# Kernel tuning notes

Measured on AMD Instinct MI355X. Metric: run time of the kernel, lower is better.

The kernel has to match this reference:

```python
import jax, jax.numpy as jnp
import numpy as np

B, S, D, U = 32, 2048, 1024, 1024


def setup_inputs() -> dict:
    key = jax.random.key(0)
    ks = jax.random.split(key, 8)
    scale_in = 1.0 / np.sqrt(D)
    scale_u = 1.0 / np.sqrt(U)
    return {
        "query": jax.random.normal(ks[0], (B, D), dtype=jnp.float32),
        "values": jax.random.normal(ks[1], (B, S, D), dtype=jnp.float32),
        "W1": jax.random.normal(ks[2], (D, U), dtype=jnp.float32) * scale_in,
        "b1": jnp.zeros((U,), dtype=jnp.float32),
        "W2": jax.random.normal(ks[3], (D, U), dtype=jnp.float32) * scale_in,
        "b2": jnp.zeros((U,), dtype=jnp.float32),
        "V": jax.random.normal(ks[4], (U, 1), dtype=jnp.float32) * scale_u,
        "bV": jnp.zeros((1,), dtype=jnp.float32),
    }


def reference(query, values, W1, b1, W2, b2, V, bV):
    # values: [B, S, D] -> [B, S, U]; query: [B, D] -> [B, 1, U]
    proj_v = jnp.einsum("bsd,du->bsu", values, W1) + b1
    proj_q = (query @ W2 + b2)[:, None, :]
    # score: [B, S, 1]
    score = jnp.einsum("bsu,uo->bso", jnp.tanh(proj_v + proj_q), V) + bV
    attention_weights = jax.nn.softmax(score, axis=1)
    # context: [B, D]
    context_vector = jnp.sum(attention_weights * values, axis=1)
    return (context_vector, attention_weights)
```

## Files before the change

kernel.cpp:

```cpp
#include <hip/hip_runtime.h>

#define DEVFN __device__ __forceinline__
#define GLOBAL_AS __attribute__((address_space(1)))
#define LDS_AS __attribute__((address_space(3)))

typedef __attribute__((ext_vector_type(4))) float f32x4;
typedef __attribute__((ext_vector_type(8))) short short8;
typedef __attribute__((ext_vector_type(8))) unsigned short ushort8;

constexpr int CB = 32;
constexpr int CS = 2048;
constexpr int CD = 1024;
constexpr int CU = 1024;
constexpr int CM = CB * CS;

DEVFN unsigned f2bf_u(float f) {
    unsigned u = __float_as_uint(f);
    return (u + 0x7FFFu + ((u >> 16) & 1u)) >> 16;
}
DEVFN unsigned f2bf_pack(float lo, float hi) {
    return f2bf_u(lo) | (f2bf_u(hi) << 16);
}
DEVFN float tanh_fast(float x) {
    float e = exp2f(x * 2.885390081777927f);
    return 1.0f - 2.0f * __builtin_amdgcn_rcpf(e + 1.0f);
}
DEVFN void async_lds16(const void* g, void* l) {
    __builtin_amdgcn_global_load_lds((const GLOBAL_AS unsigned int*)g,
                                     (LDS_AS unsigned int*)l, 16, 0, 0);
}

__global__ void k_bias1(const float* __restrict__ q, const float* __restrict__ W2,
                        float* __restrict__ bpart) {
    int dc = blockIdx.x, b = blockIdx.y;
    int t = threadIdx.x;
    __shared__ float qs[128];
    if (t < 128) qs[t] = q[b * CD + dc * 128 + t];
    __syncthreads();
    float acc0 = 0.f, acc1 = 0.f, acc2 = 0.f, acc3 = 0.f;
    const float* w2 = W2 + (size_t)(dc * 128) * CU + t;
#pragma unroll 4
    for (int d = 0; d < 128; ++d) {
        float qv = qs[d];
        const float* r = w2 + (size_t)d * CU;
        acc0 += qv * r[0];
        acc1 += qv * r[256];
        acc2 += qv * r[512];
        acc3 += qv * r[768];
    }
    float* o = bpart + (size_t)(b * 8 + dc) * CU + t;
    o[0] = acc0; o[256] = acc1; o[512] = acc2; o[768] = acc3;
}

__global__ void k_bias2(const float* __restrict__ bpart, const float* __restrict__ b1,
                        const float* __restrict__ b2, float* __restrict__ bias) {
    int idx = blockIdx.x * 256 + threadIdx.x;
    int b = idx >> 10, u = idx & 1023;
    float s = b1[u] + b2[u];
#pragma unroll
    for (int dc = 0; dc < 8; ++dc) s += bpart[(size_t)(b * 8 + dc) * CU + u];
    bias[idx] = s;
}

__global__ void k_packW1(const float* __restrict__ W1, unsigned short* __restrict__ W1p) {
    int tid = blockIdx.x * 256 + threadIdx.x;
    int o8  = tid * 8;
    int l   = (o8 >> 3) & 63;
    int ub  = (o8 >> 9) & 15;
    int ut  = (o8 >> 13) & 3;
    int kt  = o8 >> 15;
    int u  = ut * 256 + ub * 16 + (l & 15);
    int d0 = kt * 32 + (l >> 4) * 8;
    ushort8 v;
#pragma unroll
    for (int j = 0; j < 8; ++j)
        v[j] = (unsigned short)f2bf_u(W1[(size_t)(d0 + j) * CU + u]);
    *(ushort8*)(W1p + o8) = v;
}

__global__ __launch_bounds__(512, 2) void k_score(
    const float* __restrict__ values, const unsigned short* __restrict__ W1p,
    const float* __restrict__ bias, const float* __restrict__ V,
    float* __restrict__ score) {
    __shared__ __align__(16) char smem[139264];

    const int t = threadIdx.x;
    const int w = t >> 6, l = t & 63;
    const int w8 = w * 8;
    const int m0 = blockIdx.x * 64;
    const int bb = m0 >> 11;

    const float* aSrcT = values + (size_t)(m0 + (t >> 3)) * CD + (t & 7) * 4;
    const int aWrByte = (t >> 7) * 1024
                      + (((t >> 3) & 15) | (((t >> 1) & 3) << 4)) * 16
                      + (t & 1) * 8;
    const unsigned short* bSrc = W1p + (size_t)w8 * 512 + l * 8;
    const int bRdBase = (w >> 1) * 16384 + (w & 1) * 8192;

    f32x4 zero4 = {0.f, 0.f, 0.f, 0.f};
    f32x4 acc[4][8];
#pragma unroll
    for (int i = 0; i < 4; ++i)
#pragma unroll
        for (int j = 0; j < 8; ++j) acc[i][j] = zero4;

    f32x4 aH0, aH1;

    {
        char* bl = smem + 8192 + w8 * 1024;
#pragma unroll
        for (int q = 0; q < 8; ++q) async_lds16(bSrc + q * 512, bl + q * 1024);
        aH0 = *(const f32x4*)(aSrcT);
        aH1 = *(const f32x4*)(aSrcT + 32);
        uint2 pk;
        pk.x = f2bf_pack(aH0[0], aH0[1]);
        pk.y = f2bf_pack(aH0[2], aH0[3]);
        *(uint2*)(smem + aWrByte) = pk;
    }

#define SCORE_BODY(KT, AH_LD, AH_WR, DO_LD, DO_STAGE, DO_WR)                        \
    {                                                                               \
        const int cur = (KT) & 1, nxt = cur ^ 1;                                    \
        asm volatile("s_waitcnt vmcnt(1)" ::: "memory");                            \
        asm volatile("s_waitcnt lgkmcnt(0)" ::: "memory");                          \
        asm volatile("s_barrier" ::: "memory");                                     \
        __builtin_amdgcn_sched_barrier(0);                                          \
        if (DO_STAGE) {                                                             \
            const unsigned short* bs = bSrc + (size_t)((KT) + 1) * 32768;           \
            char* bl = smem + 8192 + nxt * 65536 + w8 * 1024;                       \
            _Pragma("unroll")                                                       \
            for (int q = 0; q < 8; ++q) async_lds16(bs + q * 512, bl + q * 1024);   \
        }                                                                           \
        if (DO_LD) AH_LD = *(const f32x4*)(aSrcT + ((KT) + 2) * 32);                \
        __builtin_amdgcn_sched_barrier(0);                                          \
        const char* aB = smem + cur * 4096;                                         \
        const char* bB = smem + 8192 + cur * 65536 + bRdBase;                       \
        short8 aF[4], bF[8];                                                        \
        _Pragma("unroll")                                                           \
        for (int i = 0; i < 4; ++i)                                                 \
            aF[i] = *(const short8*)(aB + i * 1024 + l * 16);                       \
        _Pragma("unroll")                                                           \
        for (int j = 0; j < 8; ++j)                                                 \
            bF[j] = *(const short8*)(bB + j * 1024 + l * 16);                       \
        __builtin_amdgcn_s_setprio(1);                                              \
        _Pragma("unroll")                                                           \
        for (int i = 0; i < 4; ++i)                                                 \
            _Pragma("unroll")                                                       \
            for (int j = 0; j < 8; ++j)                                             \
                acc[i][j] = __builtin_amdgcn_mfma_f32_16x16x32_bf16(                \
                    aF[i], bF[j], acc[i][j], 0, 0, 0);                              \
        __builtin_amdgcn_s_setprio(0);                                              \
        __builtin_amdgcn_sched_barrier(0);                                          \
        if (DO_WR) {                                                                \
            uint2 pk;                                                               \
            pk.x = f2bf_pack(AH_WR[0], AH_WR[1]);                                   \
            pk.y = f2bf_pack(AH_WR[2], AH_WR[3]);                                   \
            *(uint2*)(smem + nxt * 4096 + aWrByte) = pk;                            \
        }                                                                           \
    }

    for (int kt = 0; kt < 30; kt += 2) {
        SCORE_BODY(kt,     aH0, aH1, true, true, true)
        SCORE_BODY(kt + 1, aH1, aH0, true, true, true)
    }
    SCORE_BODY(30, aH0, aH1, false, true, true)
    SCORE_BODY(31, aH0, aH0, false, false, false)
#undef SCORE_BODY

    float part[4][4];
#pragma unroll
    for (int i = 0; i < 4; ++i)
#pragma unroll
        for (int rr = 0; rr < 4; ++rr) part[i][rr] = 0.f;

#pragma unroll
    for (int j = 0; j < 8; ++j) {
        int col = w * 128 + j * 16 + (l & 15);
        float vv = V[col];
        float bz = bias[bb * CU + col];
#pragma unroll
        for (int i = 0; i < 4; ++i)
#pragma unroll
            for (int rr = 0; rr < 4; ++rr)
                part[i][rr] += vv * tanh_fast(acc[i][j][rr] + bz);
    }

    __syncthreads();
    float* red = (float*)smem;
#pragma unroll
    for (int i = 0; i < 4; ++i)
#pragma unroll
        for (int rr = 0; rr < 4; ++rr) {
            float v = part[i][rr];
            v += __shfl_xor(v, 1);
            v += __shfl_xor(v, 2);
            v += __shfl_xor(v, 4);
            v += __shfl_xor(v, 8);
            if ((l & 15) == 0)
                red[w * 64 + i * 16 + (l >> 4) * 4 + rr] = v;
        }
    __syncthreads();
    if (t < 64) {
        float s = 0.f;
#pragma unroll
        for (int ww = 0; ww < 8; ++ww) s += red[ww * 64 + t];
        score[m0 + t] = s;
    }
}

__global__ void k_softmax(const float* __restrict__ score, float* __restrict__ wts) {
    int b = blockIdx.x, t = threadIdx.x;
    int i0 = b * CS + t, i1 = i0 + 1024;
    float s0 = score[i0];
    float s1 = score[i1];
    __shared__ float red[16];
    int wv = t >> 6, ln = t & 63;
    float m = fmaxf(s0, s1);
#pragma unroll
    for (int o = 32; o >= 1; o >>= 1) m = fmaxf(m, __shfl_xor(m, o));
    if (ln == 0) red[wv] = m;
    __syncthreads();
    float M = red[0];
#pragma unroll
    for (int k = 1; k < 16; ++k) M = fmaxf(M, red[k]);
    float e0 = __expf(s0 - M), e1 = __expf(s1 - M);
    float sm = e0 + e1;
#pragma unroll
    for (int o = 32; o >= 1; o >>= 1) sm += __shfl_xor(sm, o);
    __syncthreads();
    if (ln == 0) red[wv] = sm;
    __syncthreads();
    float T = 0.f;
#pragma unroll
    for (int k = 0; k < 16; ++k) T += red[k];
    float inv = 1.0f / T;
    wts[i0] = e0 * inv;
    wts[i1] = e1 * inv;
}

__global__ void k_ctx_part(const float* __restrict__ values, const float* __restrict__ wts,
                           float* __restrict__ part) {
    int b = blockIdx.y, sc = blockIdx.x;
    int t = threadIdx.x;
    const float* vb = values + ((size_t)b * CS + sc * 64) * CD + t * 4;
    const float* wb = wts + b * CS + sc * 64;
    f32x4 a = {0.f, 0.f, 0.f, 0.f};
#pragma unroll 8
    for (int s = 0; s < 64; ++s) {
        float wgt = wb[s];
        f32x4 v = *(const f32x4*)(vb + (size_t)s * CD);
        a += v * wgt;
    }
    *(f32x4*)(part + (size_t)(b * 32 + sc) * CD + t * 4) = a;
}

__global__ void k_ctx_red(const float* __restrict__ part, float* __restrict__ ctx) {
    int idx = blockIdx.x * 256 + threadIdx.x;
    int b = idx >> 10, d = idx & 1023;
    float s = 0.f;
#pragma unroll 8
    for (int c = 0; c < 32; ++c) s += part[(size_t)(b * 32 + c) * CD + d];
    ctx[idx] = s;
}

extern "C" void kernel_launch(void* const* d_in, const int* in_sizes, int n_in,
                              void* d_out, int out_size, void* d_ws, size_t ws_size,
                              hipStream_t stream) {
    const float* query  = (const float*)d_in[0];
    const float* values = (const float*)d_in[1];
    const float* W1     = (const float*)d_in[2];
    const float* b1     = (const float*)d_in[3];
    const float* W2     = (const float*)d_in[4];
    const float* b2     = (const float*)d_in[5];
    const float* V      = (const float*)d_in[6];

    float* out = (float*)d_out;
    float* ctx = out;
    float* wts = out + 32768;

    char* ws = (char*)d_ws;
    float*          score = (float*)ws;
    float*          bias  = (float*)(ws + (1 << 20));
    unsigned short* W1p   = (unsigned short*)(ws + (1 << 20) + (1 << 17));
    float*          part  = (float*)(ws + (1 << 20) + (1 << 17) + (1 << 21));
    float*          bpart = part;

    k_bias1<<<dim3(8, 32), 256, 0, stream>>>(query, W2, bpart);
    k_bias2<<<128, 256, 0, stream>>>(bpart, b1, b2, bias);
    k_packW1<<<512, 256, 0, stream>>>(W1, W1p);
    k_score<<<1024, 512, 0, stream>>>(values, W1p, bias, V, score);
    k_softmax<<<32, 1024, 0, stream>>>(score, wts);
    k_ctx_part<<<dim3(32, 32), 256, 0, stream>>>(values, wts, part);
    k_ctx_red<<<128, 256, 0, stream>>>(part, ctx);
}
```

Before: 268.5 us.

## Load W1 fragments directly into registers instead of staging through LDS

The B-operand (packed bf16 W1) fragments are now loaded from global memory straight into double-buffered register arrays, rather than being copied asynchronously into a 128KB LDS double buffer and read back. This shrinks shared memory to 8KB, removes the LDS round trip and the explicit vmcnt waits, and could allow more resident blocks. In exchange, each wave loads its own W1 slice from global/L2 without sharing, register pressure rises from holding two sets of eight short8 fragments, and the compiler now manages the wait counts on the global loads.

```diff
diff --git a/kernel.cpp b/kernel.cpp
--- a/kernel.cpp
+++ b/kernel.cpp
@@ -24,10 +24,6 @@
 DEVFN float tanh_fast(float x) {
     float e = exp2f(x * 2.885390081777927f);
     return 1.0f - 2.0f * __builtin_amdgcn_rcpf(e + 1.0f);
-}
-DEVFN void async_lds16(const void* g, void* l) {
-    __builtin_amdgcn_global_load_lds((const GLOBAL_AS unsigned int*)g,
-                                     (LDS_AS unsigned int*)l, 16, 0, 0);
 }
 
 __global__ void k_bias1(const float* __restrict__ q, const float* __restrict__ W2,
@@ -82,11 +78,10 @@
     const float* __restrict__ values, const unsigned short* __restrict__ W1p,
     const float* __restrict__ bias, const float* __restrict__ V,
     float* __restrict__ score) {
-    __shared__ __align__(16) char smem[139264];
+    __shared__ __align__(16) char smem[8192];
 
     const int t = threadIdx.x;
     const int w = t >> 6, l = t & 63;
-    const int w8 = w * 8;
     const int m0 = blockIdx.x * 64;
     const int bb = m0 >> 11;
 
@@ -94,8 +89,7 @@
     const int aWrByte = (t >> 7) * 1024
                       + (((t >> 3) & 15) | (((t >> 1) & 3) << 4)) * 16
                       + (t & 1) * 8;
-    const unsigned short* bSrc = W1p + (size_t)w8 * 512 + l * 8;
-    const int bRdBase = (w >> 1) * 16384 + (w & 1) * 8192;
+    const unsigned short* bSrc = W1p + (size_t)w * 4096 + l * 8;
 
     f32x4 zero4 = {0.f, 0.f, 0.f, 0.f};
     f32x4 acc[4][8];
@@ -104,67 +98,61 @@
 #pragma unroll
         for (int j = 0; j < 8; ++j) acc[i][j] = zero4;
 
+    short8 bFA[8], bFB[8];
     f32x4 aH0, aH1;
 
     {
-        char* bl = smem + 8192 + w8 * 1024;
-#pragma unroll
-        for (int q = 0; q < 8; ++q) async_lds16(bSrc + q * 512, bl + q * 1024);
+#pragma unroll
+        for (int jj = 0; jj < 8; ++jj)
+            bFA[jj] = *(const short8*)(bSrc + jj * 512);
         aH0 = *(const f32x4*)(aSrcT);
         aH1 = *(const f32x4*)(aSrcT + 32);
         uint2 pk;
         pk.x = f2bf_pack(aH0[0], aH0[1]);
         pk.y = f2bf_pack(aH0[2], aH0[3]);
         *(uint2*)(smem + aWrByte) = pk;
-    }
-
-#define SCORE_BODY(KT, AH_LD, AH_WR, DO_LD, DO_STAGE, DO_WR)                        \
+        asm volatile("s_waitcnt lgkmcnt(0)" ::: "memory");
+        asm volatile("s_barrier" ::: "memory");
+    }
+
+#define SCORE_BODY(KT, BF_CUR, BF_NXT, AH_LD, AH_WR, DO_LDB, DO_LDA, DO_WR)        \
     {                                                                               \
-        const int cur = (KT) & 1, nxt = cur ^ 1;                                    \
-        asm volatile("s_waitcnt vmcnt(1)" ::: "memory");                            \
-        asm volatile("s_waitcnt lgkmcnt(0)" ::: "memory");                          \
-        asm volatile("s_barrier" ::: "memory");                                     \
-        __builtin_amdgcn_sched_barrier(0);                                          \
-        if (DO_STAGE) {                                                             \
+        if (DO_LDB) {                                                               \
             const unsigned short* bs = bSrc + (size_t)((KT) + 1) * 32768;           \
-            char* bl = smem + 8192 + nxt * 65536 + w8 * 1024;                       \
             _Pragma("unroll")                                                       \
-            for (int q = 0; q < 8; ++q) async_lds16(bs + q * 512, bl + q * 1024);   \
+            for (int jj = 0; jj < 8; ++jj)                                          \
+                BF_NXT[jj] = *(const short8*)(bs + jj * 512);                       \
         }                                                                           \
-        if (DO_LD) AH_LD = *(const f32x4*)(aSrcT + ((KT) + 2) * 32);                \
-        __builtin_amdgcn_sched_barrier(0);                                          \
-        const char* aB = smem + cur * 4096;                                         \
-        const char* bB = smem + 8192 + cur * 65536 + bRdBase;                       \
-        short8 aF[4], bF[8];                                                        \
+        if (DO_LDA) AH_LD = *(const f32x4*)(aSrcT + ((KT) + 2) * 32);               \
+        const char* aB = smem + ((KT) & 1) * 4096;                                  \
+        short8 aF[4];                                                               \
         _Pragma("unroll")                                                           \
         for (int i = 0; i < 4; ++i)                                                 \
             aF[i] = *(const short8*)(aB + i * 1024 + l * 16);                       \
-        _Pragma("unroll")                                                           \
-        for (int j = 0; j < 8; ++j)                                                 \
-            bF[j] = *(const short8*)(bB + j * 1024 + l * 16);                       \
         __builtin_amdgcn_s_setprio(1);                                              \
         _Pragma("unroll")                                                           \
         for (int i = 0; i < 4; ++i)                                                 \
             _Pragma("unroll")                                                       \
             for (int j = 0; j < 8; ++j)                                             \
                 acc[i][j] = __builtin_amdgcn_mfma_f32_16x16x32_bf16(                \
-                    aF[i], bF[j], acc[i][j], 0, 0, 0);                              \
+                    aF[i], BF_CUR[j], acc[i][j], 0, 0, 0);                          \
         __builtin_amdgcn_s_setprio(0);                                              \
-        __builtin_amdgcn_sched_barrier(0);                                          \
         if (DO_WR) {                                                                \
             uint2 pk;                                                               \
             pk.x = f2bf_pack(AH_WR[0], AH_WR[1]);                                   \
             pk.y = f2bf_pack(AH_WR[2], AH_WR[3]);                                   \
-            *(uint2*)(smem + nxt * 4096 + aWrByte) = pk;                            \
+            *(uint2*)(smem + (((KT) + 1) & 1) * 4096 + aWrByte) = pk;               \
         }                                                                           \
+        asm volatile("s_waitcnt lgkmcnt(0)" ::: "memory");                          \
+        asm volatile("s_barrier" ::: "memory");                                     \
     }
 
     for (int kt = 0; kt < 30; kt += 2) {
-        SCORE_BODY(kt,     aH0, aH1, true, true, true)
-        SCORE_BODY(kt + 1, aH1, aH0, true, true, true)
-    }
-    SCORE_BODY(30, aH0, aH1, false, true, true)
-    SCORE_BODY(31, aH0, aH0, false, false, false)
+        SCORE_BODY(kt,     bFA, bFB, aH0, aH1, 1, 1, 1)
+        SCORE_BODY(kt + 1, bFB, bFA, aH1, aH0, 1, 1, 1)
+    }
+    SCORE_BODY(30, bFA, bFB, aH0, aH1, 1, 0, 1)
+    SCORE_BODY(31, bFB, bFA, aH1, aH0, 0, 0, 0)
 #undef SCORE_BODY
 
     float part[4][4];
```

Result: faster. 235.8 us (-12.2%).
